# Kernel tuning notes

Measured on AMD Instinct MI355X. Metric: run time of the kernel, lower is better.

The kernel has to match this reference:

```python
import jax, jax.numpy as jnp
import numpy as np

B, S, D, E, K = 2, 2048, 512, 8, 2
H = 4 * D  # 2048


def setup_inputs() -> dict:
    key = jax.random.key(0)
    ks = jax.random.split(key, 6)
    x = jax.random.normal(ks[0], (B, S, D), dtype=jnp.float32)
    # parameters, matching torch init (randn weights, zero biases)
    w1 = jax.random.normal(ks[1], (E, D, H), dtype=jnp.float32)
    w2 = jax.random.normal(ks[2], (E, H, D), dtype=jnp.float32)
    b1 = jnp.zeros((E, H), dtype=jnp.float32)
    b2 = jnp.zeros((E, D), dtype=jnp.float32)
    # nn.Linear(D, E): kaiming-uniform-ish; plain uniform is fine for a baseline
    lim = 1.0 / np.sqrt(D)
    router_w = jax.random.uniform(ks[3], (D, E), dtype=jnp.float32, minval=-lim, maxval=lim)
    router_b = jax.random.uniform(ks[4], (E,), dtype=jnp.float32, minval=-lim, maxval=lim)
    return {"x": x, "w1": w1, "w2": w2, "b1": b1, "b2": b2,
            "router_w": router_w, "router_b": router_b}


def reference(x, w1, w2, b1, b2, router_w, router_b):
    # router: [b,s,e]
    router_logits = jnp.einsum('bsd,de->bse', x, router_w) + router_b
    top_k_logits, top_k_indices = jax.lax.top_k(router_logits, K)   # [b,s,k]
    top_k_probs = jax.nn.softmax(top_k_logits, axis=-1)             # [b,s,k]
    masks = jax.nn.one_hot(top_k_indices, E, dtype=x.dtype)          # [b,s,k,e]
    # dense all-expert MLP (faithful to source: every expert on every token)
    h = jnp.einsum('bsd,edh->bseh', x, w1) + b1                      # [b,s,e,4d]
    h = jax.nn.gelu(h, approximate=False)                            # exact gelu
    y = jnp.einsum('bseh,ehd->bsed', h, w2) + b2                     # [b,s,e,d]
    # combine: mask each expert output by routed prob and sum over top-k
    out = jnp.einsum('bsed,bske,bsk->bsd', y, masks, top_k_probs)    # [b,s,d]
    return out
```

## Files before the change

kernel.cpp:

```cpp
#include <hip/hip_runtime.h>
#include <math.h>

typedef unsigned short u16;
typedef __bf16 bf16x8 __attribute__((ext_vector_type(8)));
typedef float f32x4 __attribute__((ext_vector_type(4)));

#define T_TOKENS 4096
#define D_DIM    512
#define H_DIM    2048
#define E_NUM    8
#define CAP      4096
#define NSLOT    (T_TOKENS * 2)
#define NCHUNK   16

__device__ __forceinline__ u16 f2bf(float f) {
  unsigned int u = __builtin_bit_cast(unsigned int, f);
  u = (u + 0x7fffu + ((u >> 16) & 1u)) >> 16;
  return (u16)u;
}

__device__ __forceinline__ void gload16(const void* g, void* l) {
  __builtin_amdgcn_global_load_lds(
      (__attribute__((address_space(1))) void*)(g),
      (__attribute__((address_space(3))) void*)(l), 16, 0, 0);
}

__device__ __forceinline__ float gelu_fast(float v) {
  float u = v * __fmaf_rn(0.071354817f, v * v, 1.59576912f);
  float e = __expf(-u);
  return v * __builtin_amdgcn_rcpf(1.0f + e);
}

__global__ __launch_bounds__(256) void transpose_both_kernel(const float* __restrict__ w1,
                                                             const float* __restrict__ w2,
                                                             u16* __restrict__ w1t,
                                                             u16* __restrict__ w2t) {
  __shared__ float tile[64][67];
  int bid = blockIdx.x;
  const float* in; u16* out; int R, C;
  if (bid < 2048) { in = w1; out = w1t; R = D_DIM; C = H_DIM; }
  else            { bid -= 2048; in = w2; out = w2t; R = H_DIM; C = D_DIM; }
  const int e = bid >> 8;
  const int t = bid & 255;
  const int nCx = C >> 6;
  const int c0 = (t % nCx) * 64, r0 = (t / nCx) * 64;
  const float* src = in + (size_t)e * D_DIM * H_DIM;
  u16* dst = out + (size_t)e * D_DIM * H_DIM;
  const int tid = threadIdx.x;
  {
    const int row = tid >> 2, cc = (tid & 3) * 16;
    const float* s = src + (size_t)(r0 + row) * C + c0 + cc;
#pragma unroll
    for (int j = 0; j < 4; j++)
      *(float4*)(&tile[row][cc + 4 * j]) = *(const float4*)(s + 4 * j);
  }
  __syncthreads();
  {
    const int c = tid >> 2, rc = (tid & 3) * 16;
    u16 buf[16];
#pragma unroll
    for (int j = 0; j < 16; j++) buf[j] = f2bf(tile[rc + j][c]);
    u16* d = dst + (size_t)(c0 + c) * R + r0 + rc;
    *(uint4*)(d)     = *(uint4*)(&buf[0]);
    *(uint4*)(d + 8) = *(uint4*)(&buf[8]);
  }
}

__global__ __launch_bounds__(256) void router_kernel(const float* __restrict__ x,
                                                     const float* __restrict__ rw,
                                                     const float* __restrict__ rb,
                                                     int* __restrict__ topk_idx,
                                                     float* __restrict__ topk_p,
                                                     u16* __restrict__ xb,
                                                     float* __restrict__ outz) {
  {
    float4 z = {0.f, 0.f, 0.f, 0.f};
    float4* o = (float4*)(outz + (size_t)blockIdx.x * 2048);
    o[threadIdx.x] = z;
    o[threadIdx.x + 256] = z;
  }
  const int lane = threadIdx.x & 63;
  const int t = blockIdx.x * 4 + (threadIdx.x >> 6);
  const float* xr = x + (size_t)t * D_DIM + lane * 8;
  float xv[8];
  *(float4*)(&xv[0]) = *(const float4*)(xr);
  *(float4*)(&xv[4]) = *(const float4*)(xr + 4);
  ushort4 o0, o1;
  o0.x = f2bf(xv[0]); o0.y = f2bf(xv[1]); o0.z = f2bf(xv[2]); o0.w = f2bf(xv[3]);
  o1.x = f2bf(xv[4]); o1.y = f2bf(xv[5]); o1.z = f2bf(xv[6]); o1.w = f2bf(xv[7]);
  ushort4* xo = (ushort4*)(xb + (size_t)t * D_DIM + lane * 8);
  xo[0] = o0; xo[1] = o1;

  float acc[8] = {0.f,0.f,0.f,0.f,0.f,0.f,0.f,0.f};
#pragma unroll
  for (int j = 0; j < 8; j++) {
    const float4* w = (const float4*)(rw + (size_t)(lane * 8 + j) * E_NUM);
    float4 w0 = w[0], w1 = w[1];
    acc[0] += xv[j] * w0.x; acc[1] += xv[j] * w0.y;
    acc[2] += xv[j] * w0.z; acc[3] += xv[j] * w0.w;
    acc[4] += xv[j] * w1.x; acc[5] += xv[j] * w1.y;
    acc[6] += xv[j] * w1.z; acc[7] += xv[j] * w1.w;
  }
#pragma unroll
  for (int off = 32; off > 0; off >>= 1) {
#pragma unroll
    for (int e = 0; e < 8; e++) acc[e] += __shfl_down(acc[e], off);
  }
  if (lane == 0) {
    float l[8];
#pragma unroll
    for (int e = 0; e < 8; e++) l[e] = acc[e] + rb[e];
    int i0 = 0; float v0 = l[0];
#pragma unroll
    for (int e = 1; e < 8; e++) if (l[e] > v0) { v0 = l[e]; i0 = e; }
    int i1 = -1; float v1 = -3.4e38f;
#pragma unroll
    for (int e = 0; e < 8; e++) if (e != i0 && l[e] > v1) { v1 = l[e]; i1 = e; }
    float p1 = expf(v1 - v0);
    float s = 1.0f + p1;
    topk_idx[t * 2] = i0; topk_idx[t * 2 + 1] = i1;
    topk_p[t * 2] = 1.0f / s; topk_p[t * 2 + 1] = p1 / s;
  }
}

__global__ __launch_bounds__(256) void count_kernel(const int* __restrict__ topk_idx,
                                                    int* __restrict__ chunkcnt) {
  const int b = blockIdx.x, tid = threadIdx.x, lane = tid & 63, w = tid >> 6;
  const int t = b * 256 + tid;
  const int i0 = topk_idx[t * 2], i1 = topk_idx[t * 2 + 1];
  __shared__ int ws[4][E_NUM];
#pragma unroll
  for (int e = 0; e < E_NUM; e++) {
    unsigned long long m = __ballot(i0 == e || i1 == e);
    if (lane == 0) ws[w][e] = (int)__popcll(m);
  }
  __syncthreads();
  if (tid < E_NUM)
    chunkcnt[b * E_NUM + tid] = ws[0][tid] + ws[1][tid] + ws[2][tid] + ws[3][tid];
}

__global__ __launch_bounds__(256) void scatter_kernel(const int* __restrict__ topk_idx,
                                                      const float* __restrict__ topk_p,
                                                      const int* __restrict__ chunkcnt,
                                                      int* __restrict__ slot_list,
                                                      float* __restrict__ prob_list,
                                                      int* __restrict__ counts) {
  const int e = blockIdx.x & 7, chunk = blockIdx.x >> 3;
  const int tid = threadIdx.x, lane = tid & 63, w = tid >> 6;
  int base = 0;
  for (int c = 0; c < chunk; ++c) base += chunkcnt[c * E_NUM + e];
  const int t = chunk * 256 + tid;
  const int i0 = topk_idx[t * 2], i1 = topk_idx[t * 2 + 1];
  int flag = 0, slot = 0; float p = 0.f;
  if (i0 == e)      { flag = 1; slot = t * 2;     p = topk_p[t * 2]; }
  else if (i1 == e) { flag = 1; slot = t * 2 + 1; p = topk_p[t * 2 + 1]; }
  unsigned long long m = __ballot(flag);
  __shared__ int wsum[4];
  if (lane == 0) wsum[w] = (int)__popcll(m);
  const int wpre = (int)__popcll(m & ((1ull << lane) - 1ull));
  __syncthreads();
  int wb = base;
#pragma unroll
  for (int j = 0; j < 4; j++) if (j < w) wb += wsum[j];
  if (flag) { slot_list[e * CAP + wb + wpre] = slot; prob_list[e * CAP + wb + wpre] = p; }
  if (chunk == NCHUNK - 1 && tid == 0)
    counts[e] = base + wsum[0] + wsum[1] + wsum[2] + wsum[3];
}

__global__ __launch_bounds__(256, 3) void gemm1_kernel(const u16* __restrict__ xb,
                                                       const u16* __restrict__ w1t,
                                                       const float* __restrict__ b1,
                                                       const int* __restrict__ slot_list,
                                                       const float* __restrict__ prob_list,
                                                       const int* __restrict__ counts,
                                                       u16* __restrict__ hbufc) {
  const int e  = blockIdx.x & 7;
  const int g  = blockIdx.x >> 3;
  const int cx = g & 15;
  const int rt = g >> 4;
  const int cnt = counts[e];
  const int rbase = rt * 64;
  if (rbase >= cnt) return;
  int ebase = 0;
#pragma unroll
  for (int j = 0; j < E_NUM; j++) if (j < e) ebase += counts[j];
  const int n0 = cx * 128;

  __shared__ __align__(16) u16 At[2][64 * 64];
  __shared__ __align__(16) u16 Bt[2][128 * 64];

  const int tid = threadIdx.x, lane = tid & 63, wid = tid >> 6;
  const int wr = wid >> 1, wc = wid & 1;
  const int lr8 = lane >> 3;
  const int sx = lane & 7;
  const int kperm = (sx ^ lr8) * 8;
  const int lrow = lane & 15, lk = lane >> 4;

  const u16* pa[2]; int loa[2];
#pragma unroll
  for (int i = 0; i < 2; i++) {
    const int row = (wid * 2 + i) * 8 + lr8;
    const int grow = rbase + row;
    int tok = 0;
    if (grow < cnt) tok = slot_list[e * CAP + grow] >> 1;
    pa[i] = xb + (size_t)tok * D_DIM + kperm;
    loa[i] = (wid * 2 + i) * 512;
  }
  const u16* pb[4]; int lob[4];
#pragma unroll
  for (int i = 0; i < 4; i++) {
    const int row = (wid * 4 + i) * 8 + lr8;
    pb[i] = w1t + ((size_t)e * H_DIM + n0 + row) * D_DIM + kperm;
    lob[i] = (wid * 4 + i) * 512;
  }

  f32x4 acc[2][4];
#pragma unroll
  for (int i = 0; i < 2; i++)
#pragma unroll
    for (int j = 0; j < 4; j++) acc[i][j] = (f32x4){0.f, 0.f, 0.f, 0.f};

  auto stage = [&](int k0, int b) {
#pragma unroll
    for (int i = 0; i < 2; i++) gload16(pa[i] + k0, &At[b][loa[i]]);
#pragma unroll
    for (int i = 0; i < 4; i++) gload16(pb[i] + k0, &Bt[b][lob[i]]);
  };

  stage(0, 0);
  const int nt = D_DIM / 64;
  int cur = 0;
  for (int t = 0; t < nt; ++t) {
    asm volatile("s_waitcnt vmcnt(0)" ::: "memory");
    __builtin_amdgcn_sched_barrier(0);
    __builtin_amdgcn_s_barrier();
    if (t + 1 < nt) stage((t + 1) * 64, cur ^ 1);
    bf16x8 afr[2][2], bfr[4][2];
#pragma unroll
    for (int ks = 0; ks < 2; ks++) {
#pragma unroll
      for (int fq = 0; fq < 2; fq++)
        afr[fq][ks] = *(const bf16x8*)(&At[cur][(wr * 32 + fq * 16 + lrow) * 64 + ((ks * 4 + lk) ^ sx) * 8]);
#pragma unroll
      for (int fq = 0; fq < 4; fq++)
        bfr[fq][ks] = *(const bf16x8*)(&Bt[cur][(wc * 64 + fq * 16 + lrow) * 64 + ((ks * 4 + lk) ^ sx) * 8]);
    }
    asm volatile("s_waitcnt lgkmcnt(0)" ::: "memory");
    __builtin_amdgcn_sched_barrier(0);
    __builtin_amdgcn_s_setprio(1);
#pragma unroll
    for (int ks = 0; ks < 2; ks++)
#pragma unroll
      for (int fr = 0; fr < 2; fr++)
#pragma unroll
        for (int fc = 0; fc < 4; fc++)
          acc[fr][fc] = __builtin_amdgcn_mfma_f32_16x16x32_bf16(afr[fr][ks], bfr[fc][ks], acc[fr][fc], 0, 0, 0);
    __builtin_amdgcn_s_setprio(0);
    cur ^= 1;
  }

  float bias[4];
#pragma unroll
  for (int fc = 0; fc < 4; fc++) bias[fc] = b1[e * H_DIM + n0 + wc * 64 + fc * 16 + lrow];
#pragma unroll
  for (int fr = 0; fr < 2; fr++) {
#pragma unroll
    for (int reg = 0; reg < 4; reg++) {
      const int rloc = wr * 32 + fr * 16 + lk * 4 + reg;
      const int grow = rbase + rloc;
      if (grow < cnt) {
        const float p = prob_list[e * CAP + grow];
        u16* dst = hbufc + (size_t)(ebase + grow) * H_DIM + n0 + wc * 64 + lrow;
#pragma unroll
        for (int fc = 0; fc < 4; fc++) {
          float v = acc[fr][fc][reg] + bias[fc];
          dst[fc * 16] = f2bf(gelu_fast(v) * p);
        }
      }
    }
  }
}

__global__ __launch_bounds__(256, 3) void gemm2_kernel(const u16* __restrict__ hbufc,
                                                       const u16* __restrict__ w2t,
                                                       const float* __restrict__ b2,
                                                       const int* __restrict__ slot_list,
                                                       const float* __restrict__ prob_list,
                                                       const int* __restrict__ counts,
                                                       float* __restrict__ out) {
  const int e  = blockIdx.x & 7;
  const int g  = blockIdx.x >> 3;
  const int cx = g & 3;
  const int s  = (g >> 2) & 1;
  const int rt = g >> 3;
  const int cnt = counts[e];
  const int rbase = rt * 64;
  if (rbase >= cnt) return;
  int ebase = 0;
#pragma unroll
  for (int j = 0; j < E_NUM; j++) if (j < e) ebase += counts[j];
  const int n0 = cx * 128;
  const int kb = s * (H_DIM / 2);

  __shared__ __align__(16) u16 At[2][64 * 64];
  __shared__ __align__(16) u16 Bt[2][128 * 64];

  const int tid = threadIdx.x, lane = tid & 63, wid = tid >> 6;
  const int wr = wid >> 1, wc = wid & 1;
  const int lr8 = lane >> 3;
  const int sx = lane & 7;
  const int kperm = (sx ^ lr8) * 8;
  const int lrow = lane & 15, lk = lane >> 4;

  const u16* pa[2]; int loa[2];
#pragma unroll
  for (int i = 0; i < 2; i++) {
    const int row = (wid * 2 + i) * 8 + lr8;
    const int grow = rbase + row;
    const int cr = (grow < cnt) ? (ebase + grow) : 0;
    pa[i] = hbufc + (size_t)cr * H_DIM + kb + kperm;
    loa[i] = (wid * 2 + i) * 512;
  }
  const u16* pb[4]; int lob[4];
#pragma unroll
  for (int i = 0; i < 4; i++) {
    const int row = (wid * 4 + i) * 8 + lr8;
    pb[i] = w2t + ((size_t)e * D_DIM + n0 + row) * H_DIM + kb + kperm;
    lob[i] = (wid * 4 + i) * 512;
  }

  f32x4 acc[2][4];
#pragma unroll
  for (int i = 0; i < 2; i++)
#pragma unroll
    for (int j = 0; j < 4; j++) acc[i][j] = (f32x4){0.f, 0.f, 0.f, 0.f};

  auto stage = [&](int k0, int b) {
#pragma unroll
    for (int i = 0; i < 2; i++) gload16(pa[i] + k0, &At[b][loa[i]]);
#pragma unroll
    for (int i = 0; i < 4; i++) gload16(pb[i] + k0, &Bt[b][lob[i]]);
  };

  stage(0, 0);
  const int nt = (H_DIM / 2) / 64;
  int cur = 0;
  for (int t = 0; t < nt; ++t) {
    asm volatile("s_waitcnt vmcnt(0)" ::: "memory");
    __builtin_amdgcn_sched_barrier(0);
    __builtin_amdgcn_s_barrier();
    if (t + 1 < nt) stage((t + 1) * 64, cur ^ 1);
    bf16x8 afr[2][2], bfr[4][2];
#pragma unroll
    for (int ks = 0; ks < 2; ks++) {
#pragma unroll
      for (int fq = 0; fq < 2; fq++)
        afr[fq][ks] = *(const bf16x8*)(&At[cur][(wr * 32 + fq * 16 + lrow) * 64 + ((ks * 4 + lk) ^ sx) * 8]);
#pragma unroll
      for (int fq = 0; fq < 4; fq++)
        bfr[fq][ks] = *(const bf16x8*)(&Bt[cur][(wc * 64 + fq * 16 + lrow) * 64 + ((ks * 4 + lk) ^ sx) * 8]);
    }
    asm volatile("s_waitcnt lgkmcnt(0)" ::: "memory");
    __builtin_amdgcn_sched_barrier(0);
    __builtin_amdgcn_s_setprio(1);
#pragma unroll
    for (int ks = 0; ks < 2; ks++)
#pragma unroll
      for (int fr = 0; fr < 2; fr++)
#pragma unroll
        for (int fc = 0; fc < 4; fc++)
          acc[fr][fc] = __builtin_amdgcn_mfma_f32_16x16x32_bf16(afr[fr][ks], bfr[fc][ks], acc[fr][fc], 0, 0, 0);
    __builtin_amdgcn_s_setprio(0);
    cur ^= 1;
  }

#pragma unroll
  for (int fr = 0; fr < 2; fr++) {
#pragma unroll
    for (int reg = 0; reg < 4; reg++) {
      const int rloc = wr * 32 + fr * 16 + lk * 4 + reg;
      const int grow = rbase + rloc;
      if (grow < cnt) {
        const int slot = slot_list[e * CAP + grow];
        const float p  = prob_list[e * CAP + grow];
        float* dst = out + (size_t)(slot >> 1) * D_DIM + n0 + wc * 64 + lrow;
#pragma unroll
        for (int fc = 0; fc < 4; fc++) {
          float v = acc[fr][fc][reg];
          if (s == 0) v += p * b2[e * D_DIM + n0 + wc * 64 + fc * 16 + lrow];
          atomicAdd(&dst[fc * 16], v);
        }
      }
    }
  }
}

extern "C" void kernel_launch(void* const* d_in, const int* in_sizes, int n_in,
                              void* d_out, int out_size, void* d_ws, size_t ws_size,
                              hipStream_t stream) {
  const float* x  = (const float*)d_in[0];
  const float* w1 = (const float*)d_in[1];
  const float* w2 = (const float*)d_in[2];
  const float* b1 = (const float*)d_in[3];
  const float* b2 = (const float*)d_in[4];
  const float* rw = (const float*)d_in[5];
  const float* rb = (const float*)d_in[6];
  float* out = (float*)d_out;

  char* ws = (char*)d_ws;
  size_t off = 0;
  auto alloc = [&](size_t bytes) -> void* {
    void* p = ws + off;
    off = (off + bytes + 255) & ~(size_t)255;
    return p;
  };
  int*   counts    = (int*)alloc(E_NUM * 4);
  int*   chunkcnt  = (int*)alloc(NCHUNK * E_NUM * 4);
  int*   slot_list = (int*)alloc((size_t)E_NUM * CAP * 4);
  float* prob_list = (float*)alloc((size_t)E_NUM * CAP * 4);
  int*   topk_idx  = (int*)alloc((size_t)T_TOKENS * 2 * 4);
  float* topk_p    = (float*)alloc((size_t)T_TOKENS * 2 * 4);
  u16*   xb        = (u16*)alloc((size_t)T_TOKENS * D_DIM * 2);
  u16*   w1t       = (u16*)alloc((size_t)E_NUM * H_DIM * D_DIM * 2);
  u16*   w2t       = (u16*)alloc((size_t)E_NUM * H_DIM * D_DIM * 2);
  u16*   hbufc     = (u16*)alloc((size_t)NSLOT * H_DIM * 2);

  transpose_both_kernel<<<4096, 256, 0, stream>>>(w1, w2, w1t, w2t);
  router_kernel<<<T_TOKENS / 4, 256, 0, stream>>>(x, rw, rb, topk_idx, topk_p, xb, out);
  count_kernel<<<NCHUNK, 256, 0, stream>>>(topk_idx, chunkcnt);
  scatter_kernel<<<NCHUNK * E_NUM, 256, 0, stream>>>(topk_idx, topk_p, chunkcnt, slot_list, prob_list, counts);
  gemm1_kernel<<<E_NUM * 16 * 64, 256, 0, stream>>>(xb, w1t, b1, slot_list, prob_list, counts, hbufc);
  gemm2_kernel<<<E_NUM * 4 * 2 * 64, 256, 0, stream>>>(hbufc, w2t, b2, slot_list, prob_list, counts, out);
}
```

Measured before the change: 125.0 us.

## Use 256x256 tiles with 8-wave pipelined schedule in gemm1; drop split-K in gemm2

gemm1 moves from 64x128 tiles with 4 waves to 256x256 tiles with 8 waves (512 threads). It uses a depth-2 prefetch with partial vmcnt waits and interleaves A/B staging between MFMA quarter-blocks, which raises operand reuse and overlaps loads with compute. gemm2 no longer splits K in two, so it issues half the atomic adds at the cost of fewer blocks and longer loops. Risks include lower occupancy, padding waste when an expert's count is not a multiple of 256 rows, and register pressure from 32 accumulators per thread.

```diff
diff --git a/kernel.cpp b/kernel.cpp
--- a/kernel.cpp
+++ b/kernel.cpp
@@ -167,7 +167,7 @@
     counts[e] = base + wsum[0] + wsum[1] + wsum[2] + wsum[3];
 }
 
-__global__ __launch_bounds__(256, 3) void gemm1_kernel(const u16* __restrict__ xb,
+__global__ __launch_bounds__(512, 1) void gemm1_kernel(const u16* __restrict__ xb,
                                                        const u16* __restrict__ w1t,
                                                        const float* __restrict__ b1,
                                                        const int* __restrict__ slot_list,
@@ -176,105 +176,139 @@
                                                        u16* __restrict__ hbufc) {
   const int e  = blockIdx.x & 7;
   const int g  = blockIdx.x >> 3;
-  const int cx = g & 15;
-  const int rt = g >> 4;
+  const int cx = g & 7;
+  const int rt = g >> 3;
   const int cnt = counts[e];
-  const int rbase = rt * 64;
+  const int rbase = rt * 256;
   if (rbase >= cnt) return;
   int ebase = 0;
 #pragma unroll
   for (int j = 0; j < E_NUM; j++) if (j < e) ebase += counts[j];
-  const int n0 = cx * 128;
-
-  __shared__ __align__(16) u16 At[2][64 * 64];
-  __shared__ __align__(16) u16 Bt[2][128 * 64];
+  const int n0 = cx * 256;
+
+  __shared__ __align__(16) u16 At[2][256 * 64];
+  __shared__ __align__(16) u16 Bt[2][256 * 64];
 
   const int tid = threadIdx.x, lane = tid & 63, wid = tid >> 6;
-  const int wr = wid >> 1, wc = wid & 1;
-  const int lr8 = lane >> 3;
-  const int sx = lane & 7;
-  const int kperm = (sx ^ lr8) * 8;
+  const int wm = wid >> 2, wn = wid & 3;
   const int lrow = lane & 15, lk = lane >> 4;
 
-  const u16* pa[2]; int loa[2];
-#pragma unroll
-  for (int i = 0; i < 2; i++) {
-    const int row = (wid * 2 + i) * 8 + lr8;
+  const u16* pA[4]; const u16* pB[4]; int lofs[4];
+#pragma unroll
+  for (int j = 0; j < 4; j++) {
+    const int gch = j * 512 + tid;
+    const int row = gch >> 3, c = gch & 7;
+    const int ck = (c ^ (row & 7)) << 3;
     const int grow = rbase + row;
     int tok = 0;
     if (grow < cnt) tok = slot_list[e * CAP + grow] >> 1;
-    pa[i] = xb + (size_t)tok * D_DIM + kperm;
-    loa[i] = (wid * 2 + i) * 512;
-  }
-  const u16* pb[4]; int lob[4];
-#pragma unroll
-  for (int i = 0; i < 4; i++) {
-    const int row = (wid * 4 + i) * 8 + lr8;
-    pb[i] = w1t + ((size_t)e * H_DIM + n0 + row) * D_DIM + kperm;
-    lob[i] = (wid * 4 + i) * 512;
-  }
-
-  f32x4 acc[2][4];
-#pragma unroll
-  for (int i = 0; i < 2; i++)
+    pA[j] = xb + (size_t)tok * D_DIM + ck;
+    pB[j] = w1t + ((size_t)e * H_DIM + n0 + row) * D_DIM + ck;
+    lofs[j] = gch << 3;
+  }
+
+  int aoff[8][2], boff[4][2];
+#pragma unroll
+  for (int mf = 0; mf < 8; mf++) {
+    const int r = wm * 128 + mf * 16 + lrow;
+#pragma unroll
+    for (int ks = 0; ks < 2; ks++)
+      aoff[mf][ks] = r * 64 + (((ks * 4 + lk) ^ (r & 7)) << 3);
+  }
+#pragma unroll
+  for (int nf = 0; nf < 4; nf++) {
+    const int r = wn * 64 + nf * 16 + lrow;
+#pragma unroll
+    for (int ks = 0; ks < 2; ks++)
+      boff[nf][ks] = r * 64 + (((ks * 4 + lk) ^ (r & 7)) << 3);
+  }
+
+  f32x4 acc[8][4];
+#pragma unroll
+  for (int i = 0; i < 8; i++)
 #pragma unroll
     for (int j = 0; j < 4; j++) acc[i][j] = (f32x4){0.f, 0.f, 0.f, 0.f};
 
-  auto stage = [&](int k0, int b) {
-#pragma unroll
-    for (int i = 0; i < 2; i++) gload16(pa[i] + k0, &At[b][loa[i]]);
-#pragma unroll
-    for (int i = 0; i < 4; i++) gload16(pb[i] + k0, &Bt[b][lob[i]]);
-  };
-
-  stage(0, 0);
+  auto stageA = [&](int T) { const int s = T & 1; const int k0 = T * 64;
+#pragma unroll
+    for (int j = 0; j < 4; j++) gload16(pA[j] + k0, &At[s][lofs[j]]); };
+  auto stageB = [&](int T) { const int s = T & 1; const int k0 = T * 64;
+#pragma unroll
+    for (int j = 0; j < 4; j++) gload16(pB[j] + k0, &Bt[s][lofs[j]]); };
+
+  stageA(0); stageB(0); stageA(1); stageB(1);
   const int nt = D_DIM / 64;
-  int cur = 0;
-  for (int t = 0; t < nt; ++t) {
-    asm volatile("s_waitcnt vmcnt(0)" ::: "memory");
+  for (int T = 0; T < nt; ++T) {
+    const int s = T & 1;
+    if (T < nt - 1) { asm volatile("s_waitcnt vmcnt(8)" ::: "memory"); }
+    else            { asm volatile("s_waitcnt vmcnt(0)" ::: "memory"); }
     __builtin_amdgcn_sched_barrier(0);
     __builtin_amdgcn_s_barrier();
-    if (t + 1 < nt) stage((t + 1) * 64, cur ^ 1);
-    bf16x8 afr[2][2], bfr[4][2];
-#pragma unroll
-    for (int ks = 0; ks < 2; ks++) {
-#pragma unroll
-      for (int fq = 0; fq < 2; fq++)
-        afr[fq][ks] = *(const bf16x8*)(&At[cur][(wr * 32 + fq * 16 + lrow) * 64 + ((ks * 4 + lk) ^ sx) * 8]);
-#pragma unroll
-      for (int fq = 0; fq < 4; fq++)
-        bfr[fq][ks] = *(const bf16x8*)(&Bt[cur][(wc * 64 + fq * 16 + lrow) * 64 + ((ks * 4 + lk) ^ sx) * 8]);
-    }
+    bf16x8 a0[8], b0[4], a1[8], bq[4];
+#pragma unroll
+    for (int mf = 0; mf < 8; mf++) a0[mf] = *(const bf16x8*)(&At[s][aoff[mf][0]]);
+#pragma unroll
+    for (int nf = 0; nf < 4; nf++) b0[nf] = *(const bf16x8*)(&Bt[s][boff[nf][0]]);
     asm volatile("s_waitcnt lgkmcnt(0)" ::: "memory");
     __builtin_amdgcn_sched_barrier(0);
     __builtin_amdgcn_s_setprio(1);
 #pragma unroll
-    for (int ks = 0; ks < 2; ks++)
-#pragma unroll
-      for (int fr = 0; fr < 2; fr++)
-#pragma unroll
-        for (int fc = 0; fc < 4; fc++)
-          acc[fr][fc] = __builtin_amdgcn_mfma_f32_16x16x32_bf16(afr[fr][ks], bfr[fc][ks], acc[fr][fc], 0, 0, 0);
+    for (int mf = 0; mf < 4; mf++)
+#pragma unroll
+      for (int nf = 0; nf < 4; nf++)
+        acc[mf][nf] = __builtin_amdgcn_mfma_f32_16x16x32_bf16(a0[mf], b0[nf], acc[mf][nf], 0, 0, 0);
     __builtin_amdgcn_s_setprio(0);
-    cur ^= 1;
+    __builtin_amdgcn_s_barrier();
+#pragma unroll
+    for (int mf = 0; mf < 8; mf++) a1[mf] = *(const bf16x8*)(&At[s][aoff[mf][1]]);
+#pragma unroll
+    for (int nf = 0; nf < 4; nf++) bq[nf] = *(const bf16x8*)(&Bt[s][boff[nf][1]]);
+    asm volatile("s_waitcnt lgkmcnt(0)" ::: "memory");
+    __builtin_amdgcn_sched_barrier(0);
+    __builtin_amdgcn_s_setprio(1);
+#pragma unroll
+    for (int mf = 4; mf < 8; mf++)
+#pragma unroll
+      for (int nf = 0; nf < 4; nf++)
+        acc[mf][nf] = __builtin_amdgcn_mfma_f32_16x16x32_bf16(a0[mf], b0[nf], acc[mf][nf], 0, 0, 0);
+    __builtin_amdgcn_s_setprio(0);
+    __builtin_amdgcn_s_barrier();
+    if (T + 2 < nt) stageA(T + 2);
+    __builtin_amdgcn_s_setprio(1);
+#pragma unroll
+    for (int mf = 0; mf < 4; mf++)
+#pragma unroll
+      for (int nf = 0; nf < 4; nf++)
+        acc[mf][nf] = __builtin_amdgcn_mfma_f32_16x16x32_bf16(a1[mf], bq[nf], acc[mf][nf], 0, 0, 0);
+    __builtin_amdgcn_s_setprio(0);
+    __builtin_amdgcn_s_barrier();
+    if (T + 2 < nt) stageB(T + 2);
+    __builtin_amdgcn_s_setprio(1);
+#pragma unroll
+    for (int mf = 4; mf < 8; mf++)
+#pragma unroll
+      for (int nf = 0; nf < 4; nf++)
+        acc[mf][nf] = __builtin_amdgcn_mfma_f32_16x16x32_bf16(a1[mf], bq[nf], acc[mf][nf], 0, 0, 0);
+    __builtin_amdgcn_s_setprio(0);
+    __builtin_amdgcn_s_barrier();
   }
 
   float bias[4];
 #pragma unroll
-  for (int fc = 0; fc < 4; fc++) bias[fc] = b1[e * H_DIM + n0 + wc * 64 + fc * 16 + lrow];
-#pragma unroll
-  for (int fr = 0; fr < 2; fr++) {
+  for (int nf = 0; nf < 4; nf++) bias[nf] = b1[e * H_DIM + n0 + wn * 64 + nf * 16 + lrow];
+#pragma unroll
+  for (int mf = 0; mf < 8; mf++) {
 #pragma unroll
     for (int reg = 0; reg < 4; reg++) {
-      const int rloc = wr * 32 + fr * 16 + lk * 4 + reg;
+      const int rloc = wm * 128 + mf * 16 + lk * 4 + reg;
       const int grow = rbase + rloc;
       if (grow < cnt) {
         const float p = prob_list[e * CAP + grow];
-        u16* dst = hbufc + (size_t)(ebase + grow) * H_DIM + n0 + wc * 64 + lrow;
-#pragma unroll
-        for (int fc = 0; fc < 4; fc++) {
-          float v = acc[fr][fc][reg] + bias[fc];
-          dst[fc * 16] = f2bf(gelu_fast(v) * p);
+        u16* dst = hbufc + (size_t)(ebase + grow) * H_DIM + n0 + wn * 64 + lrow;
+#pragma unroll
+        for (int nf = 0; nf < 4; nf++) {
+          float v = acc[mf][nf][reg] + bias[nf];
+          dst[nf * 16] = f2bf(gelu_fast(v) * p);
         }
       }
     }
@@ -291,8 +325,7 @@
   const int e  = blockIdx.x & 7;
   const int g  = blockIdx.x >> 3;
   const int cx = g & 3;
-  const int s  = (g >> 2) & 1;
-  const int rt = g >> 3;
+  const int rt = g >> 2;
   const int cnt = counts[e];
   const int rbase = rt * 64;
   if (rbase >= cnt) return;
@@ -300,7 +333,6 @@
 #pragma unroll
   for (int j = 0; j < E_NUM; j++) if (j < e) ebase += counts[j];
   const int n0 = cx * 128;
-  const int kb = s * (H_DIM / 2);
 
   __shared__ __align__(16) u16 At[2][64 * 64];
   __shared__ __align__(16) u16 Bt[2][128 * 64];
@@ -318,14 +350,14 @@
     const int row = (wid * 2 + i) * 8 + lr8;
     const int grow = rbase + row;
     const int cr = (grow < cnt) ? (ebase + grow) : 0;
-    pa[i] = hbufc + (size_t)cr * H_DIM + kb + kperm;
+    pa[i] = hbufc + (size_t)cr * H_DIM + kperm;
     loa[i] = (wid * 2 + i) * 512;
   }
   const u16* pb[4]; int lob[4];
 #pragma unroll
   for (int i = 0; i < 4; i++) {
     const int row = (wid * 4 + i) * 8 + lr8;
-    pb[i] = w2t + ((size_t)e * D_DIM + n0 + row) * H_DIM + kb + kperm;
+    pb[i] = w2t + ((size_t)e * D_DIM + n0 + row) * H_DIM + kperm;
     lob[i] = (wid * 4 + i) * 512;
   }
 
@@ -343,7 +375,7 @@
   };
 
   stage(0, 0);
-  const int nt = (H_DIM / 2) / 64;
+  const int nt = H_DIM / 64;
   int cur = 0;
   for (int t = 0; t < nt; ++t) {
     asm volatile("s_waitcnt vmcnt(0)" ::: "memory");
@@ -386,8 +418,7 @@
         float* dst = out + (size_t)(slot >> 1) * D_DIM + n0 + wc * 64 + lrow;
 #pragma unroll
         for (int fc = 0; fc < 4; fc++) {
-          float v = acc[fr][fc][reg];
-          if (s == 0) v += p * b2[e * D_DIM + n0 + wc * 64 + fc * 16 + lrow];
+          float v = acc[fr][fc][reg] + p * b2[e * D_DIM + n0 + wc * 64 + fc * 16 + lrow];
           atomicAdd(&dst[fc * 16], v);
         }
       }
@@ -429,6 +460,6 @@
   router_kernel<<<T_TOKENS / 4, 256, 0, stream>>>(x, rw, rb, topk_idx, topk_p, xb, out);
   count_kernel<<<NCHUNK, 256, 0, stream>>>(topk_idx, chunkcnt);
   scatter_kernel<<<NCHUNK * E_NUM, 256, 0, stream>>>(topk_idx, topk_p, chunkcnt, slot_list, prob_list, counts);
-  gemm1_kernel<<<E_NUM * 16 * 64, 256, 0, stream>>>(xb, w1t, b1, slot_list, prob_list, counts, hbufc);
-  gemm2_kernel<<<E_NUM * 4 * 2 * 64, 256, 0, stream>>>(hbufc, w2t, b2, slot_list, prob_list, counts, out);
-}
+  gemm1_kernel<<<E_NUM * 16 * 8, 512, 0, stream>>>(xb, w1t, b1, slot_list, prob_list, counts, hbufc);
+  gemm2_kernel<<<E_NUM * 4 * 64, 256, 0, stream>>>(hbufc, w2t, b2, slot_list, prob_list, counts, out);
+}
```

New measurement: 120.6 us. 1.04x faster.

## Load A operands directly into registers, enlarge gemm1 M tile, drop gemm2 split-K

Applied to the files above, without the earlier changes.

Both grouped GEMMs now read the gathered A rows straight from global memory into registers in MFMA fragment layout, bypassing LDS. Only the weight (B) tile is still staged through double-buffered LDS. gemm1 doubles its row tile to 128, so each B tile serves more tokens. gemm2 drops its 2-way split-K, which halves the atomic adds on the output but gives fewer blocks and longer K loops. Register pressure rises, and the uncoalesced per-lane A loads may expose global latency.

```diff
diff --git a/kernel.cpp b/kernel.cpp
--- a/kernel.cpp
+++ b/kernel.cpp
@@ -179,102 +179,112 @@
   const int cx = g & 15;
   const int rt = g >> 4;
   const int cnt = counts[e];
-  const int rbase = rt * 64;
+  const int rbase = rt * 128;
   if (rbase >= cnt) return;
   int ebase = 0;
 #pragma unroll
   for (int j = 0; j < E_NUM; j++) if (j < e) ebase += counts[j];
   const int n0 = cx * 128;
 
-  __shared__ __align__(16) u16 At[2][64 * 64];
   __shared__ __align__(16) u16 Bt[2][128 * 64];
 
   const int tid = threadIdx.x, lane = tid & 63, wid = tid >> 6;
   const int wr = wid >> 1, wc = wid & 1;
-  const int lr8 = lane >> 3;
-  const int sx = lane & 7;
-  const int kperm = (sx ^ lr8) * 8;
   const int lrow = lane & 15, lk = lane >> 4;
 
-  const u16* pa[2]; int loa[2];
-#pragma unroll
-  for (int i = 0; i < 2; i++) {
-    const int row = (wid * 2 + i) * 8 + lr8;
-    const int grow = rbase + row;
+  const u16* aptr[4];
+#pragma unroll
+  for (int mf = 0; mf < 4; mf++) {
+    const int r = rbase + wr * 64 + mf * 16 + lrow;
     int tok = 0;
-    if (grow < cnt) tok = slot_list[e * CAP + grow] >> 1;
-    pa[i] = xb + (size_t)tok * D_DIM + kperm;
-    loa[i] = (wid * 2 + i) * 512;
-  }
+    if (r < cnt) tok = slot_list[e * CAP + r] >> 1;
+    aptr[mf] = xb + (size_t)tok * D_DIM + lk * 8;
+  }
+
   const u16* pb[4]; int lob[4];
 #pragma unroll
-  for (int i = 0; i < 4; i++) {
-    const int row = (wid * 4 + i) * 8 + lr8;
-    pb[i] = w1t + ((size_t)e * H_DIM + n0 + row) * D_DIM + kperm;
-    lob[i] = (wid * 4 + i) * 512;
-  }
-
-  f32x4 acc[2][4];
-#pragma unroll
-  for (int i = 0; i < 2; i++)
+  for (int j = 0; j < 4; j++) {
+    const int gch = j * 256 + tid;
+    const int row = gch >> 3, c = gch & 7;
+    const int ck = (c ^ (row & 7)) << 3;
+    pb[j] = w1t + ((size_t)e * H_DIM + n0 + row) * D_DIM + ck;
+    lob[j] = gch << 3;
+  }
+
+  int boff[4][2];
+#pragma unroll
+  for (int nf = 0; nf < 4; nf++) {
+    const int r = wc * 64 + nf * 16 + lrow;
+#pragma unroll
+    for (int ks = 0; ks < 2; ks++)
+      boff[nf][ks] = r * 64 + (((ks * 4 + lk) ^ (r & 7)) << 3);
+  }
+
+  f32x4 acc[4][4];
+#pragma unroll
+  for (int i = 0; i < 4; i++)
 #pragma unroll
     for (int j = 0; j < 4; j++) acc[i][j] = (f32x4){0.f, 0.f, 0.f, 0.f};
 
-  auto stage = [&](int k0, int b) {
-#pragma unroll
-    for (int i = 0; i < 2; i++) gload16(pa[i] + k0, &At[b][loa[i]]);
-#pragma unroll
-    for (int i = 0; i < 4; i++) gload16(pb[i] + k0, &Bt[b][lob[i]]);
-  };
-
-  stage(0, 0);
+  auto stageB = [&](int t) { const int s = t & 1; const int k0 = t * 64;
+#pragma unroll
+    for (int j = 0; j < 4; j++) gload16(pb[j] + k0, &Bt[s][lob[j]]); };
+
+  uint4 areg[4][2];
+  auto loadA = [&](int t) { const int k0 = t * 64;
+#pragma unroll
+    for (int mf = 0; mf < 4; mf++) {
+      areg[mf][0] = *(const uint4*)(aptr[mf] + k0);
+      areg[mf][1] = *(const uint4*)(aptr[mf] + k0 + 32);
+    } };
+
+  stageB(0);
+  loadA(0);
   const int nt = D_DIM / 64;
-  int cur = 0;
   for (int t = 0; t < nt; ++t) {
+    const int s = t & 1;
     asm volatile("s_waitcnt vmcnt(0)" ::: "memory");
     __builtin_amdgcn_sched_barrier(0);
     __builtin_amdgcn_s_barrier();
-    if (t + 1 < nt) stage((t + 1) * 64, cur ^ 1);
-    bf16x8 afr[2][2], bfr[4][2];
+    if (t + 1 < nt) stageB(t + 1);
+    bf16x8 bfr[4][2];
+#pragma unroll
+    for (int nf = 0; nf < 4; nf++) {
+      bfr[nf][0] = *(const bf16x8*)(&Bt[s][boff[nf][0]]);
+      bfr[nf][1] = *(const bf16x8*)(&Bt[s][boff[nf][1]]);
+    }
+    __builtin_amdgcn_s_setprio(1);
 #pragma unroll
     for (int ks = 0; ks < 2; ks++) {
-#pragma unroll
-      for (int fq = 0; fq < 2; fq++)
-        afr[fq][ks] = *(const bf16x8*)(&At[cur][(wr * 32 + fq * 16 + lrow) * 64 + ((ks * 4 + lk) ^ sx) * 8]);
-#pragma unroll
-      for (int fq = 0; fq < 4; fq++)
-        bfr[fq][ks] = *(const bf16x8*)(&Bt[cur][(wc * 64 + fq * 16 + lrow) * 64 + ((ks * 4 + lk) ^ sx) * 8]);
-    }
-    asm volatile("s_waitcnt lgkmcnt(0)" ::: "memory");
-    __builtin_amdgcn_sched_barrier(0);
-    __builtin_amdgcn_s_setprio(1);
-#pragma unroll
-    for (int ks = 0; ks < 2; ks++)
-#pragma unroll
-      for (int fr = 0; fr < 2; fr++)
-#pragma unroll
-        for (int fc = 0; fc < 4; fc++)
-          acc[fr][fc] = __builtin_amdgcn_mfma_f32_16x16x32_bf16(afr[fr][ks], bfr[fc][ks], acc[fr][fc], 0, 0, 0);
+      bf16x8 av[4];
+#pragma unroll
+      for (int mf = 0; mf < 4; mf++) av[mf] = __builtin_bit_cast(bf16x8, areg[mf][ks]);
+#pragma unroll
+      for (int mf = 0; mf < 4; mf++)
+#pragma unroll
+        for (int nf = 0; nf < 4; nf++)
+          acc[mf][nf] = __builtin_amdgcn_mfma_f32_16x16x32_bf16(av[mf], bfr[nf][ks], acc[mf][nf], 0, 0, 0);
+    }
     __builtin_amdgcn_s_setprio(0);
-    cur ^= 1;
+    if (t + 1 < nt) loadA(t + 1);
   }
 
   float bias[4];
 #pragma unroll
-  for (int fc = 0; fc < 4; fc++) bias[fc] = b1[e * H_DIM + n0 + wc * 64 + fc * 16 + lrow];
-#pragma unroll
-  for (int fr = 0; fr < 2; fr++) {
+  for (int nf = 0; nf < 4; nf++) bias[nf] = b1[e * H_DIM + n0 + wc * 64 + nf * 16 + lrow];
+#pragma unroll
+  for (int mf = 0; mf < 4; mf++) {
 #pragma unroll
     for (int reg = 0; reg < 4; reg++) {
-      const int rloc = wr * 32 + fr * 16 + lk * 4 + reg;
+      const int rloc = wr * 64 + mf * 16 + lk * 4 + reg;
       const int grow = rbase + rloc;
       if (grow < cnt) {
         const float p = prob_list[e * CAP + grow];
         u16* dst = hbufc + (size_t)(ebase + grow) * H_DIM + n0 + wc * 64 + lrow;
 #pragma unroll
-        for (int fc = 0; fc < 4; fc++) {
-          float v = acc[fr][fc][reg] + bias[fc];
-          dst[fc * 16] = f2bf(gelu_fast(v) * p);
+        for (int nf = 0; nf < 4; nf++) {
+          float v = acc[mf][nf][reg] + bias[nf];
+          dst[nf * 16] = f2bf(gelu_fast(v) * p);
         }
       }
     }
@@ -291,8 +301,7 @@
   const int e  = blockIdx.x & 7;
   const int g  = blockIdx.x >> 3;
   const int cx = g & 3;
-  const int s  = (g >> 2) & 1;
-  const int rt = g >> 3;
+  const int rt = g >> 2;
   const int cnt = counts[e];
   const int rbase = rt * 64;
   if (rbase >= cnt) return;
@@ -300,33 +309,38 @@
 #pragma unroll
   for (int j = 0; j < E_NUM; j++) if (j < e) ebase += counts[j];
   const int n0 = cx * 128;
-  const int kb = s * (H_DIM / 2);
-
-  __shared__ __align__(16) u16 At[2][64 * 64];
+
   __shared__ __align__(16) u16 Bt[2][128 * 64];
 
   const int tid = threadIdx.x, lane = tid & 63, wid = tid >> 6;
   const int wr = wid >> 1, wc = wid & 1;
-  const int lr8 = lane >> 3;
-  const int sx = lane & 7;
-  const int kperm = (sx ^ lr8) * 8;
   const int lrow = lane & 15, lk = lane >> 4;
 
-  const u16* pa[2]; int loa[2];
-#pragma unroll
-  for (int i = 0; i < 2; i++) {
-    const int row = (wid * 2 + i) * 8 + lr8;
-    const int grow = rbase + row;
-    const int cr = (grow < cnt) ? (ebase + grow) : 0;
-    pa[i] = hbufc + (size_t)cr * H_DIM + kb + kperm;
-    loa[i] = (wid * 2 + i) * 512;
-  }
+  const u16* aptr[2];
+#pragma unroll
+  for (int mf = 0; mf < 2; mf++) {
+    const int r = rbase + wr * 32 + mf * 16 + lrow;
+    const int cr = (r < cnt) ? (ebase + r) : 0;
+    aptr[mf] = hbufc + (size_t)cr * H_DIM + lk * 8;
+  }
+
   const u16* pb[4]; int lob[4];
 #pragma unroll
-  for (int i = 0; i < 4; i++) {
-    const int row = (wid * 4 + i) * 8 + lr8;
-    pb[i] = w2t + ((size_t)e * D_DIM + n0 + row) * H_DIM + kb + kperm;
-    lob[i] = (wid * 4 + i) * 512;
+  for (int j = 0; j < 4; j++) {
+    const int gch = j * 256 + tid;
+    const int row = gch >> 3, c = gch & 7;
+    const int ck = (c ^ (row & 7)) << 3;
+    pb[j] = w2t + ((size_t)e * D_DIM + n0 + row) * H_DIM + ck;
+    lob[j] = gch << 3;
+  }
+
+  int boff[4][2];
+#pragma unroll
+  for (int nf = 0; nf < 4; nf++) {
+    const int r = wc * 64 + nf * 16 + lrow;
+#pragma unroll
+    for (int ks = 0; ks < 2; ks++)
+      boff[nf][ks] = r * 64 + (((ks * 4 + lk) ^ (r & 7)) << 3);
   }
 
   f32x4 acc[2][4];
@@ -335,60 +349,63 @@
 #pragma unroll
     for (int j = 0; j < 4; j++) acc[i][j] = (f32x4){0.f, 0.f, 0.f, 0.f};
 
-  auto stage = [&](int k0, int b) {
-#pragma unroll
-    for (int i = 0; i < 2; i++) gload16(pa[i] + k0, &At[b][loa[i]]);
-#pragma unroll
-    for (int i = 0; i < 4; i++) gload16(pb[i] + k0, &Bt[b][lob[i]]);
-  };
-
-  stage(0, 0);
-  const int nt = (H_DIM / 2) / 64;
-  int cur = 0;
+  auto stageB = [&](int t) { const int s = t & 1; const int k0 = t * 64;
+#pragma unroll
+    for (int j = 0; j < 4; j++) gload16(pb[j] + k0, &Bt[s][lob[j]]); };
+
+  uint4 areg[2][2];
+  auto loadA = [&](int t) { const int k0 = t * 64;
+#pragma unroll
+    for (int mf = 0; mf < 2; mf++) {
+      areg[mf][0] = *(const uint4*)(aptr[mf] + k0);
+      areg[mf][1] = *(const uint4*)(aptr[mf] + k0 + 32);
+    } };
+
+  stageB(0);
+  loadA(0);
+  const int nt = H_DIM / 64;
   for (int t = 0; t < nt; ++t) {
+    const int s = t & 1;
     asm volatile("s_waitcnt vmcnt(0)" ::: "memory");
     __builtin_amdgcn_sched_barrier(0);
     __builtin_amdgcn_s_barrier();
-    if (t + 1 < nt) stage((t + 1) * 64, cur ^ 1);
-    bf16x8 afr[2][2], bfr[4][2];
+    if (t + 1 < nt) stageB(t + 1);
+    bf16x8 bfr[4][2];
+#pragma unroll
+    for (int nf = 0; nf < 4; nf++) {
+      bfr[nf][0] = *(const bf16x8*)(&Bt[s][boff[nf][0]]);
+      bfr[nf][1] = *(const bf16x8*)(&Bt[s][boff[nf][1]]);
+    }
+    __builtin_amdgcn_s_setprio(1);
 #pragma unroll
     for (int ks = 0; ks < 2; ks++) {
-#pragma unroll
-      for (int fq = 0; fq < 2; fq++)
-        afr[fq][ks] = *(const bf16x8*)(&At[cur][(wr * 32 + fq * 16 + lrow) * 64 + ((ks * 4 + lk) ^ sx) * 8]);
-#pragma unroll
-      for (int fq = 0; fq < 4; fq++)
-        bfr[fq][ks] = *(const bf16x8*)(&Bt[cur][(wc * 64 + fq * 16 + lrow) * 64 + ((ks * 4 + lk) ^ sx) * 8]);
-    }
-    asm volatile("s_waitcnt lgkmcnt(0)" ::: "memory");
-    __builtin_amdgcn_sched_barrier(0);
-    __builtin_amdgcn_s_setprio(1);
-#pragma unroll
-    for (int ks = 0; ks < 2; ks++)
-#pragma unroll
-      for (int fr = 0; fr < 2; fr++)
-#pragma unroll
-        for (int fc = 0; fc < 4; fc++)
-          acc[fr][fc] = __builtin_amdgcn_mfma_f32_16x16x32_bf16(afr[fr][ks], bfr[fc][ks], acc[fr][fc], 0, 0, 0);
+      bf16x8 av[2];
+#pragma unroll
+      for (int mf = 0; mf < 2; mf++) av[mf] = __builtin_bit_cast(bf16x8, areg[mf][ks]);
+#pragma unroll
+      for (int mf = 0; mf < 2; mf++)
+#pragma unroll
+        for (int nf = 0; nf < 4; nf++)
+          acc[mf][nf] = __builtin_amdgcn_mfma_f32_16x16x32_bf16(av[mf], bfr[nf][ks], acc[mf][nf], 0, 0, 0);
+    }
     __builtin_amdgcn_s_setprio(0);
-    cur ^= 1;
-  }
-
-#pragma unroll
-  for (int fr = 0; fr < 2; fr++) {
+    if (t + 1 < nt) loadA(t + 1);
+  }
+
+#pragma unroll
+  for (int mf = 0; mf < 2; mf++) {
 #pragma unroll
     for (int reg = 0; reg < 4; reg++) {
-      const int rloc = wr * 32 + fr * 16 + lk * 4 + reg;
+      const int rloc = wr * 32 + mf * 16 + lk * 4 + reg;
       const int grow = rbase + rloc;
       if (grow < cnt) {
         const int slot = slot_list[e * CAP + grow];
         const float p  = prob_list[e * CAP + grow];
         float* dst = out + (size_t)(slot >> 1) * D_DIM + n0 + wc * 64 + lrow;
 #pragma unroll
-        for (int fc = 0; fc < 4; fc++) {
-          float v = acc[fr][fc][reg];
-          if (s == 0) v += p * b2[e * D_DIM + n0 + wc * 64 + fc * 16 + lrow];
-          atomicAdd(&dst[fc * 16], v);
+        for (int nf = 0; nf < 4; nf++) {
+          float v = acc[mf][nf][reg] + p * b2[e * D_DIM + n0 + wc * 64 + nf * 16 + lrow];
+          atomicAdd(&dst[nf * 16], v);
         }
       }
     }
@@ -429,6 +446,6 @@
   router_kernel<<<T_TOKENS / 4, 256, 0, stream>>>(x, rw, rb, topk_idx, topk_p, xb, out);
   count_kernel<<<NCHUNK, 256, 0, stream>>>(topk_idx, chunkcnt);
   scatter_kernel<<<NCHUNK * E_NUM, 256, 0, stream>>>(topk_idx, topk_p, chunkcnt, slot_list, prob_list, counts);
-  gemm1_kernel<<<E_NUM * 16 * 64, 256, 0, stream>>>(xb, w1t, b1, slot_list, prob_list, counts, hbufc);
-  gemm2_kernel<<<E_NUM * 4 * 2 * 64, 256, 0, stream>>>(hbufc, w2t, b2, slot_list, prob_list, counts, out);
-}
+  gemm1_kernel<<<E_NUM * 32 * 16, 256, 0, stream>>>(xb, w1t, b1, slot_list, prob_list, counts, hbufc);
+  gemm2_kernel<<<E_NUM * 64 * 4, 256, 0, stream>>>(hbufc, w2t, b2, slot_list, prob_list, counts, out);
+}
```

Result: slower. 162.9 us (+30.4%).

## Drop split-K in gemm2 and use 32-row tiles over full K

Applied to the files above, without the earlier changes.

gemm2 no longer splits the 2048-long K dimension into two halves. Each block now covers 32 rows by 128 columns over the full K, with the bias added once and occupancy raised to 4 blocks per SM. This halves the atomicAdd traffic into the output and removes the duplicate partial sums, and the smaller row tile keeps the block count about the same so the GPU stays filled. The cost is that each block now runs twice as many K iterations, and the smaller M tile means each B tile loaded from LDS is reused for less compute.

```diff
diff --git a/kernel.cpp b/kernel.cpp
--- a/kernel.cpp
+++ b/kernel.cpp
@@ -281,7 +281,7 @@
   }
 }
 
-__global__ __launch_bounds__(256, 3) void gemm2_kernel(const u16* __restrict__ hbufc,
+__global__ __launch_bounds__(256, 4) void gemm2_kernel(const u16* __restrict__ hbufc,
                                                        const u16* __restrict__ w2t,
                                                        const float* __restrict__ b2,
                                                        const int* __restrict__ slot_list,
@@ -291,74 +291,81 @@
   const int e  = blockIdx.x & 7;
   const int g  = blockIdx.x >> 3;
   const int cx = g & 3;
-  const int s  = (g >> 2) & 1;
-  const int rt = g >> 3;
+  const int rt = g >> 2;
   const int cnt = counts[e];
-  const int rbase = rt * 64;
+  const int rbase = rt * 32;
   if (rbase >= cnt) return;
   int ebase = 0;
 #pragma unroll
   for (int j = 0; j < E_NUM; j++) if (j < e) ebase += counts[j];
   const int n0 = cx * 128;
-  const int kb = s * (H_DIM / 2);
-
-  __shared__ __align__(16) u16 At[2][64 * 64];
+
+  __shared__ __align__(16) u16 At[2][32 * 64];
   __shared__ __align__(16) u16 Bt[2][128 * 64];
 
   const int tid = threadIdx.x, lane = tid & 63, wid = tid >> 6;
   const int wr = wid >> 1, wc = wid & 1;
-  const int lr8 = lane >> 3;
-  const int sx = lane & 7;
-  const int kperm = (sx ^ lr8) * 8;
   const int lrow = lane & 15, lk = lane >> 4;
 
-  const u16* pa[2]; int loa[2];
-#pragma unroll
-  for (int i = 0; i < 2; i++) {
-    const int row = (wid * 2 + i) * 8 + lr8;
+  const u16* pa; int loa;
+  {
+    const int row = tid >> 3, c = tid & 7;
+    const int ck = (c ^ (row & 7)) << 3;
     const int grow = rbase + row;
     const int cr = (grow < cnt) ? (ebase + grow) : 0;
-    pa[i] = hbufc + (size_t)cr * H_DIM + kb + kperm;
-    loa[i] = (wid * 2 + i) * 512;
+    pa = hbufc + (size_t)cr * H_DIM + ck;
+    loa = tid << 3;
   }
   const u16* pb[4]; int lob[4];
 #pragma unroll
-  for (int i = 0; i < 4; i++) {
-    const int row = (wid * 4 + i) * 8 + lr8;
-    pb[i] = w2t + ((size_t)e * D_DIM + n0 + row) * H_DIM + kb + kperm;
-    lob[i] = (wid * 4 + i) * 512;
-  }
-
-  f32x4 acc[2][4];
-#pragma unroll
-  for (int i = 0; i < 2; i++)
-#pragma unroll
-    for (int j = 0; j < 4; j++) acc[i][j] = (f32x4){0.f, 0.f, 0.f, 0.f};
+  for (int j = 0; j < 4; j++) {
+    const int gch = j * 256 + tid;
+    const int row = gch >> 3, c = gch & 7;
+    const int ck = (c ^ (row & 7)) << 3;
+    pb[j] = w2t + ((size_t)e * D_DIM + n0 + row) * H_DIM + ck;
+    lob[j] = gch << 3;
+  }
+
+  int aoff[2], boff[4][2];
+  {
+    const int r = wr * 16 + lrow;
+#pragma unroll
+    for (int ks = 0; ks < 2; ks++)
+      aoff[ks] = r * 64 + (((ks * 4 + lk) ^ (r & 7)) << 3);
+  }
+#pragma unroll
+  for (int nf = 0; nf < 4; nf++) {
+    const int r = wc * 64 + nf * 16 + lrow;
+#pragma unroll
+    for (int ks = 0; ks < 2; ks++)
+      boff[nf][ks] = r * 64 + (((ks * 4 + lk) ^ (r & 7)) << 3);
+  }
+
+  f32x4 acc[4];
+#pragma unroll
+  for (int j = 0; j < 4; j++) acc[j] = (f32x4){0.f, 0.f, 0.f, 0.f};
 
   auto stage = [&](int k0, int b) {
-#pragma unroll
-    for (int i = 0; i < 2; i++) gload16(pa[i] + k0, &At[b][loa[i]]);
-#pragma unroll
-    for (int i = 0; i < 4; i++) gload16(pb[i] + k0, &Bt[b][lob[i]]);
+    gload16(pa + k0, &At[b][loa]);
+#pragma unroll
+    for (int j = 0; j < 4; j++) gload16(pb[j] + k0, &Bt[b][lob[j]]);
   };
 
   stage(0, 0);
-  const int nt = (H_DIM / 2) / 64;
+  const int nt = H_DIM / 64;
   int cur = 0;
   for (int t = 0; t < nt; ++t) {
     asm volatile("s_waitcnt vmcnt(0)" ::: "memory");
     __builtin_amdgcn_sched_barrier(0);
     __builtin_amdgcn_s_barrier();
     if (t + 1 < nt) stage((t + 1) * 64, cur ^ 1);
-    bf16x8 afr[2][2], bfr[4][2];
+    bf16x8 afr[2], bfr[4][2];
 #pragma unroll
     for (int ks = 0; ks < 2; ks++) {
-#pragma unroll
-      for (int fq = 0; fq < 2; fq++)
-        afr[fq][ks] = *(const bf16x8*)(&At[cur][(wr * 32 + fq * 16 + lrow) * 64 + ((ks * 4 + lk) ^ sx) * 8]);
-#pragma unroll
-      for (int fq = 0; fq < 4; fq++)
-        bfr[fq][ks] = *(const bf16x8*)(&Bt[cur][(wc * 64 + fq * 16 + lrow) * 64 + ((ks * 4 + lk) ^ sx) * 8]);
+      afr[ks] = *(const bf16x8*)(&At[cur][aoff[ks]]);
+#pragma unroll
+      for (int nf = 0; nf < 4; nf++)
+        bfr[nf][ks] = *(const bf16x8*)(&Bt[cur][boff[nf][ks]]);
     }
     asm volatile("s_waitcnt lgkmcnt(0)" ::: "memory");
     __builtin_amdgcn_sched_barrier(0);
@@ -366,30 +373,24 @@
 #pragma unroll
     for (int ks = 0; ks < 2; ks++)
 #pragma unroll
-      for (int fr = 0; fr < 2; fr++)
-#pragma unroll
-        for (int fc = 0; fc < 4; fc++)
-          acc[fr][fc] = __builtin_amdgcn_mfma_f32_16x16x32_bf16(afr[fr][ks], bfr[fc][ks], acc[fr][fc], 0, 0, 0);
+      for (int nf = 0; nf < 4; nf++)
+        acc[nf] = __builtin_amdgcn_mfma_f32_16x16x32_bf16(afr[ks], bfr[nf][ks], acc[nf], 0, 0, 0);
     __builtin_amdgcn_s_setprio(0);
     cur ^= 1;
   }
 
 #pragma unroll
-  for (int fr = 0; fr < 2; fr++) {
-#pragma unroll
-    for (int reg = 0; reg < 4; reg++) {
-      const int rloc = wr * 32 + fr * 16 + lk * 4 + reg;
-      const int grow = rbase + rloc;
-      if (grow < cnt) {
-        const int slot = slot_list[e * CAP + grow];
-        const float p  = prob_list[e * CAP + grow];
-        float* dst = out + (size_t)(slot >> 1) * D_DIM + n0 + wc * 64 + lrow;
-#pragma unroll
-        for (int fc = 0; fc < 4; fc++) {
-          float v = acc[fr][fc][reg];
-          if (s == 0) v += p * b2[e * D_DIM + n0 + wc * 64 + fc * 16 + lrow];
-          atomicAdd(&dst[fc * 16], v);
-        }
+  for (int reg = 0; reg < 4; reg++) {
+    const int rloc = wr * 16 + lk * 4 + reg;
+    const int grow = rbase + rloc;
+    if (grow < cnt) {
+      const int slot = slot_list[e * CAP + grow];
+      const float p  = prob_list[e * CAP + grow];
+      float* dst = out + (size_t)(slot >> 1) * D_DIM + n0 + wc * 64 + lrow;
+#pragma unroll
+      for (int nf = 0; nf < 4; nf++) {
+        float v = acc[nf][reg] + p * b2[e * D_DIM + n0 + wc * 64 + nf * 16 + lrow];
+        atomicAdd(&dst[nf * 16], v);
       }
     }
   }
@@ -430,5 +431,5 @@
   count_kernel<<<NCHUNK, 256, 0, stream>>>(topk_idx, chunkcnt);
   scatter_kernel<<<NCHUNK * E_NUM, 256, 0, stream>>>(topk_idx, topk_p, chunkcnt, slot_list, prob_list, counts);
   gemm1_kernel<<<E_NUM * 16 * 64, 256, 0, stream>>>(xb, w1t, b1, slot_list, prob_list, counts, hbufc);
-  gemm2_kernel<<<E_NUM * 4 * 2 * 64, 256, 0, stream>>>(hbufc, w2t, b2, slot_list, prob_list, counts, out);
-}
+  gemm2_kernel<<<E_NUM * 4 * 128, 256, 0, stream>>>(hbufc, w2t, b2, slot_list, prob_list, counts, out);
+}
```

Measured after the change: 132.3 us. 5.9% more time.
